# Kernel optimization log

Measured on AMD Instinct MI355X. Metric: run time of the kernel, lower is better.

The kernel has to match this reference:

```python
import jax, jax.numpy as jnp
import numpy as np

B, M, R = 32768, 64, 16

def setup_inputs() -> dict:
    key = jax.random.key(0)
    # x: [B, M, R, 2] real/imag stacked, matching the torch module's input layout
    x = jax.random.normal(key, (B, M, R, 2), dtype=jnp.float32)
    return {"x": x}

def reference(x) -> jnp.ndarray:
    # Combine real/imag channels into a complex matrix per batch element.
    xc = jax.lax.complex(x[..., 0], x[..., 1])  # [B, M, R] complex64
    # Batched reduced QR (replaces the Python loop of per-batch torch.linalg.qr).
    q, _ = jnp.linalg.qr(xc, mode="reduced")    # q: [B, M, R] complex64
    # Split back into stacked real/imag channels: [B, M, R, 2]
    return jnp.stack([q.real, q.imag], axis=-1)
```

## Files before the change

kernel.cpp:

```cpp
#include <hip/hip_runtime.h>


constexpr int Mrows = 64;
constexpr int Rcols = 16;

typedef int v2i __attribute__((ext_vector_type(2)));

#if defined(__has_builtin)
#if __has_builtin(__builtin_amdgcn_permlane16_swap)
#define USE_PL16 1
#else
#define USE_PL16 0
#endif
#if __has_builtin(__builtin_amdgcn_permlane32_swap)
#define USE_PL32 1
#else
#define USE_PL32 0
#endif
#else
#define USE_PL16 0
#define USE_PL32 0
#endif

__device__ __forceinline__ float rdlane(float v, int srclane) {
  return __int_as_float(__builtin_amdgcn_readlane(__float_as_int(v), srclane));
}

__device__ __forceinline__ float plswap16_addf(float v) {
#if USE_PL16
  v2i r = __builtin_amdgcn_permlane16_swap(__float_as_int(v), __float_as_int(v),
                                           false, false);
  return __int_as_float(r[0]) + __int_as_float(r[1]);
#else
  return v + __shfl_xor(v, 16, 64);
#endif
}

__device__ __forceinline__ float plswap32_addf(float v) {
#if USE_PL32
  v2i r = __builtin_amdgcn_permlane32_swap(__float_as_int(v), __float_as_int(v),
                                           false, false);
  return __int_as_float(r[0]) + __int_as_float(r[1]);
#else
  return v + __shfl_xor(v, 32, 64);
#endif
}

template <int CTRL, int RM>
__device__ __forceinline__ double dpp_dadd(double v) {
  union { double d; int i[2]; } u, s;
  u.d = v;
  s.i[0] = __builtin_amdgcn_update_dpp(0, u.i[0], CTRL, RM, 0xF, true);
  s.i[1] = __builtin_amdgcn_update_dpp(0, u.i[1], CTRL, RM, 0xF, true);
  return v + s.d;
}

__device__ __forceinline__ double rdlaned(double v, int srclane) {
  union { double d; int i[2]; } u, r;
  u.d = v;
  r.i[0] = __builtin_amdgcn_readlane(u.i[0], srclane);
  r.i[1] = __builtin_amdgcn_readlane(u.i[1], srclane);
  return r.d;
}

__device__ __forceinline__ double wsum64d_fast(double v) {
  v = dpp_dadd<0xB1, 0xF>(v);
  v = dpp_dadd<0x4E, 0xF>(v);
  v = dpp_dadd<0x141, 0xF>(v);
  v = dpp_dadd<0x140, 0xF>(v);
  v = dpp_dadd<0x142, 0xA>(v);
  v = dpp_dadd<0x143, 0xC>(v);
  return rdlaned(v, 63);
}

__device__ void qr_f64_fused(const float* __restrict__ x,
                             float* __restrict__ out, int b, int lane) {
  const float4* xp = reinterpret_cast<const float4*>(
      x + (size_t)b * (Mrows * Rcols * 2) + (size_t)lane * (Rcols * 2));
  double xr[Rcols], xi[Rcols], ar[Rcols], ai[Rcols];
#pragma unroll
  for (int k = 0; k < Rcols / 2; ++k) {
    float4 t = xp[k];
    xr[2 * k] = (double)t.x;      xi[2 * k] = (double)t.y;
    xr[2 * k + 1] = (double)t.z;  xi[2 * k + 1] = (double)t.w;
  }
#pragma unroll
  for (int j = 0; j < Rcols; ++j) { ar[j] = xr[j]; ai[j] = xi[j]; }

#pragma unroll
  for (int i = 0; i < Rcols; ++i) {
    double cr = ar[i], ci = ai[i];
    double sq = (lane > i) ? (cr * cr + ci * ci) : 0.0;
    double xnorm2 = wsum64d_fast(sq);
    double alphr = rdlaned(cr, i);
    double alphi = rdlaned(ci, i);

    double tr, ti;
    if (xnorm2 == 0.0 && alphi == 0.0) {
      tr = 0.0;  ti = 0.0;
    } else {
      double nrm = sqrt(alphr * alphr + alphi * alphi + xnorm2);
      double beta = (alphr >= 0.0) ? -nrm : nrm;
      double rb = 1.0 / beta;
      tr = (beta - alphr) * rb;
      ti = -alphi * rb;
      double dr = alphr - beta, di = alphi;
      double inv = 1.0 / (dr * dr + di * di);
      double sr = dr * inv, si = -di * inv;
      if (lane > i) {
        double nr = cr * sr - ci * si;
        double ni = cr * si + ci * sr;
        ar[i] = nr;
        ai[i] = ni;
      }
      if (lane == i) { ar[i] = beta; ai[i] = 0.0; }
    }

    double vr = (lane == i) ? 1.0 : ((lane > i) ? ar[i] : 0.0);
    double vi = (lane == i) ? 0.0 : ((lane > i) ? ai[i] : 0.0);
    const double ctr = tr, cti = -ti;
#pragma unroll
    for (int j = i + 1; j < Rcols; ++j) {
      double pr = fma(vr, ar[j], vi * ai[j]);
      double pi = fma(vr, ai[j], -(vi * ar[j]));
      pr = wsum64d_fast(pr);
      pi = wsum64d_fast(pi);
      double wr = fma(ctr, pr, -(cti * pi));
      double wi = fma(ctr, pi, cti * pr);
      ar[j] = fma(-wr, vr, fma(wi, vi, ar[j]));
      ai[j] = fma(-wr, vi, fma(-wi, vr, ai[j]));
    }

    double swr = xr[i], swi = xi[i];
#pragma unroll
    for (int k = 0; k < Rcols; ++k) {
      if (k >= i) break;
      double rr = rdlaned(ar[i], k);
      double ri = rdlaned(ai[i], k);
      swr = fma(-xr[k], rr, fma(xi[k], ri, swr));
      swi = fma(-xr[k], ri, fma(-xi[k], rr, swi));
    }
    double rbd = 1.0 / rdlaned(ar[i], i);
    xr[i] = swr * rbd;
    xi[i] = swi * rbd;
  }

  float4* op = reinterpret_cast<float4*>(
      out + (size_t)b * (Mrows * Rcols * 2) + (size_t)lane * (Rcols * 2));
#pragma unroll
  for (int k = 0; k < Rcols / 2; ++k) {
    op[k] = make_float4((float)xr[2 * k], (float)xi[2 * k],
                        (float)xr[2 * k + 1], (float)xi[2 * k + 1]);
  }
}

template <int I>
__device__ __forceinline__ void qr_step(int lane, float (&Ar)[16], float (&Ai)[16],
                                        float (&Pr)[16], float (&Pi)[16],
                                        int bpaR, bool& risky) {
  const int c = lane & 15;
  const bool g0 = (lane < 16);

  float ahi = 0.f, alo = 0.f;
#pragma unroll
  for (int m = 0; m < 16; ++m) {
    float s = fmaf(Ar[m], Ar[m], Ai[m] * Ai[m]);
    if (m > I) ahi += s; else alo += s;
  }
  float locn = g0 ? ahi : (ahi + alo);
  locn = plswap16_addf(locn);
  locn = plswap32_addf(locn);
  float xnorm2 = rdlane(locn, I);
  float alphr = rdlane(Ar[I], I);
  float alphi = rdlane(Ai[I], I);
  risky = risky || (fabsf(alphr) < 2e-4f);

  float ctr, cti, dr, di, beta_s;
  if (xnorm2 == 0.f && alphi == 0.f) {
    ctr = 0.f; cti = 0.f; dr = 0.f; di = 0.f;
    beta_s = alphr;
  } else {
    float nrm = __builtin_amdgcn_sqrtf(
        fmaf(alphr, alphr, fmaf(alphi, alphi, xnorm2)));
    float beta = (alphr >= 0.f) ? -nrm : nrm;
    float rbeta = __builtin_amdgcn_rcpf(beta);
    float tr = (beta - alphr) * rbeta;
    float ti = -alphi * rbeta;
    dr = alphr - beta;  di = alphi;
    float inv = __builtin_amdgcn_rcpf(fmaf(dr, dr, di * di));
    ctr = tr * inv;
    cti = -(ti * inv);
    beta_s = beta;
  }
  float rbq = __builtin_amdgcn_rcpf(beta_s);

  float ur[16], ui[16];
#pragma unroll
  for (int m = 0; m < 16; ++m) {
    ur[m] = __int_as_float(__builtin_amdgcn_ds_swizzle(
        __float_as_int(Ar[m]), (I << 5) | 0x10));
    ui[m] = __int_as_float(__builtin_amdgcn_ds_swizzle(
        __float_as_int(Ai[m]), (I << 5) | 0x10));
  }
#pragma unroll
  for (int m = 0; m < I; ++m) {
    ur[m] = g0 ? 0.f : ur[m];
    ui[m] = g0 ? 0.f : ui[m];
  }
  ur[I] = g0 ? dr : ur[I];
  ui[I] = g0 ? di : ui[I];

  float pr = 0.f, pi = 0.f;
#pragma unroll
  for (int m = 0; m < 16; ++m) {
    pr = fmaf(ur[m], Ar[m], fmaf(ui[m], Ai[m], pr));
    pi = fmaf(ur[m], Ai[m], fmaf(-ui[m], Ar[m], pi));
  }
  pr = plswap16_addf(pr);  pr = plswap32_addf(pr);
  pi = plswap16_addf(pi);  pi = plswap32_addf(pi);
  const bool cle = (c <= I);
  pr = cle ? 0.f : pr;
  pi = cle ? 0.f : pi;

  float wr = fmaf(ctr, pr, -(cti * pi));
  float wi = fmaf(ctr, pi, cti * pr);
#pragma unroll
  for (int m = 0; m < 16; ++m) {
    Ar[m] = fmaf(-wr, ur[m], fmaf(wi, ui[m], Ar[m]));
    Ai[m] = fmaf(-wr, ui[m], fmaf(-wi, ur[m], Ai[m]));
  }

  float rr = __int_as_float(
      __builtin_amdgcn_ds_bpermute(bpaR, __float_as_int(Ar[I])));
  float ri = __int_as_float(
      __builtin_amdgcn_ds_bpermute(bpaR, __float_as_int(Ai[I])));
  const bool ceq = (c == I);
  const bool clt = (c < I);
  rr = ceq ? (beta_s - 1.f) : rr;
  rr = clt ? 0.f : rr;
  ri = cle ? 0.f : ri;

#pragma unroll
  for (int m = 0; m < 16; ++m) {
    ur[m] = __int_as_float(__builtin_amdgcn_ds_swizzle(
        __float_as_int(Pr[m]), (I << 5) | 0x10));
    ui[m] = __int_as_float(__builtin_amdgcn_ds_swizzle(
        __float_as_int(Pi[m]), (I << 5) | 0x10));
  }
#pragma unroll
  for (int m = 0; m < 16; ++m) {
    float qbr = ur[m] * rbq;
    float qbi = ui[m] * rbq;
    Pr[m] = fmaf(-qbr, rr, fmaf(qbi, ri, Pr[m]));
    Pi[m] = fmaf(-qbr, ri, fmaf(-qbi, rr, Pi[m]));
  }
}

__global__ __launch_bounds__(256)
__attribute__((amdgpu_waves_per_eu(3)))
void qr_fused(const float* __restrict__ x, float* __restrict__ out, int B) {
  const int lane = threadIdx.x & 63;
  const int wave = threadIdx.x >> 6;
  const int b = blockIdx.x * 4 + wave;
  if (b >= B) return;
  const int c = lane & 15;
  const int gbase = lane & 48;
  const int bpaR = c << 2;

  const float2* xp = reinterpret_cast<const float2*>(x) +
                     (size_t)b * (Mrows * Rcols) + (size_t)gbase * Rcols + c;
  float Ar[16], Ai[16], Pr[16], Pi[16];
#pragma unroll
  for (int m = 0; m < 16; ++m) {
    float2 t = xp[m * Rcols];
    Ar[m] = t.x;  Ai[m] = t.y;
    Pr[m] = t.x;  Pi[m] = t.y;
  }

  bool risky = false;
  qr_step<0>(lane, Ar, Ai, Pr, Pi, bpaR, risky);
  qr_step<1>(lane, Ar, Ai, Pr, Pi, bpaR, risky);
  qr_step<2>(lane, Ar, Ai, Pr, Pi, bpaR, risky);
  qr_step<3>(lane, Ar, Ai, Pr, Pi, bpaR, risky);
  qr_step<4>(lane, Ar, Ai, Pr, Pi, bpaR, risky);
  qr_step<5>(lane, Ar, Ai, Pr, Pi, bpaR, risky);
  qr_step<6>(lane, Ar, Ai, Pr, Pi, bpaR, risky);
  qr_step<7>(lane, Ar, Ai, Pr, Pi, bpaR, risky);
  qr_step<8>(lane, Ar, Ai, Pr, Pi, bpaR, risky);
  qr_step<9>(lane, Ar, Ai, Pr, Pi, bpaR, risky);
  qr_step<10>(lane, Ar, Ai, Pr, Pi, bpaR, risky);
  qr_step<11>(lane, Ar, Ai, Pr, Pi, bpaR, risky);
  qr_step<12>(lane, Ar, Ai, Pr, Pi, bpaR, risky);
  qr_step<13>(lane, Ar, Ai, Pr, Pi, bpaR, risky);
  qr_step<14>(lane, Ar, Ai, Pr, Pi, bpaR, risky);
  qr_step<15>(lane, Ar, Ai, Pr, Pi, bpaR, risky);

  if (risky) {
    qr_f64_fused(x, out, b, lane);
    return;
  }

  float2* op = reinterpret_cast<float2*>(out) +
               (size_t)b * (Mrows * Rcols) + (size_t)gbase * Rcols + c;
#pragma unroll
  for (int m = 0; m < 16; ++m) {
    op[m * Rcols] = make_float2(Pr[m], Pi[m]);
  }
}

extern "C" void kernel_launch(void* const* d_in, const int* in_sizes, int n_in,
                              void* d_out, int out_size, void* d_ws,
                              size_t ws_size, hipStream_t stream) {
  const float* x = (const float*)d_in[0];
  float* out = (float*)d_out;
  const int B = in_sizes[0] / (Mrows * Rcols * 2);
  dim3 block(256);
  dim3 grid((B + 3) / 4);
  qr_fused<<<grid, block, 0, stream>>>(x, out, B);
}
```

Measured before the change: 585.6 us.

## Pack QR step arithmetic into float2 FMAs and downdate column norms incrementally

Stores the per-lane matrix and Q registers as two-wide float vectors so the dot product, rank-1 update and Q update can compile to packed FMA instructions. It also replaces the per-step recomputation of the column norm (a 16-element reduction plus two cross-lane swaps) with a running column sum-of-squares. That sum is computed once up front and downdated each step by the squared R entry. The downdate can lose accuracy through cancellation, which is only partly guarded by clamping at zero and by the existing fp64 fallback.

```diff
diff --git a/kernel.cpp b/kernel.cpp
--- a/kernel.cpp
+++ b/kernel.cpp
@@ -5,6 +5,7 @@
 constexpr int Rcols = 16;
 
 typedef int v2i __attribute__((ext_vector_type(2)));
+typedef float v2f __attribute__((ext_vector_type(2)));
 
 #if defined(__has_builtin)
 #if __has_builtin(__builtin_amdgcn_permlane16_swap)
@@ -44,6 +45,24 @@
 #else
   return v + __shfl_xor(v, 32, 64);
 #endif
+}
+
+__device__ __forceinline__ v2f pkfma(v2f a, v2f b, v2f c) {
+#if defined(__has_builtin) && __has_builtin(__builtin_elementwise_fma)
+  return __builtin_elementwise_fma(a, b, c);
+#else
+  v2f r;
+  r[0] = fmaf(a[0], b[0], c[0]);
+  r[1] = fmaf(a[1], b[1], c[1]);
+  return r;
+#endif
+}
+
+__device__ __forceinline__ v2f splat2(float s) { v2f r; r[0] = s; r[1] = s; return r; }
+
+template <int IMM>
+__device__ __forceinline__ float dswz(float v) {
+  return __int_as_float(__builtin_amdgcn_ds_swizzle(__float_as_int(v), IMM));
 }
 
 template <int CTRL, int RM>
@@ -155,24 +174,21 @@
 }
 
 template <int I>
-__device__ __forceinline__ void qr_step(int lane, float (&Ar)[16], float (&Ai)[16],
-                                        float (&Pr)[16], float (&Pi)[16],
-                                        int bpaR, bool& risky) {
+__device__ __forceinline__ void qr_step(int lane,
+                                        v2f (&Ar2)[8], v2f (&Ai2)[8],
+                                        v2f (&Pr2)[8], v2f (&Pi2)[8],
+                                        float& S, int bpaR, bool& risky) {
   const int c = lane & 15;
   const bool g0 = (lane < 16);
-
-  float ahi = 0.f, alo = 0.f;
-#pragma unroll
-  for (int m = 0; m < 16; ++m) {
-    float s = fmaf(Ar[m], Ar[m], Ai[m] * Ai[m]);
-    if (m > I) ahi += s; else alo += s;
-  }
-  float locn = g0 ? ahi : (ahi + alo);
-  locn = plswap16_addf(locn);
-  locn = plswap32_addf(locn);
-  float xnorm2 = rdlane(locn, I);
-  float alphr = rdlane(Ar[I], I);
-  float alphi = rdlane(Ai[I], I);
+  constexpr int IH = I / 2;
+  constexpr int ILo = I % 2;
+  constexpr int SWZ = (I << 5) | 0x10;
+  const v2f z2 = splat2(0.f);
+
+  float alphr = rdlane(Ar2[IH][ILo], I);
+  float alphi = rdlane(Ai2[IH][ILo], I);
+  float SI = rdlane(S, I);
+  float xnorm2 = fmaxf(SI - fmaf(alphr, alphr, alphi * alphi), 0.f);
   risky = risky || (fabsf(alphr) < 2e-4f);
 
   float ctr, cti, dr, di, beta_s;
@@ -194,28 +210,39 @@
   }
   float rbq = __builtin_amdgcn_rcpf(beta_s);
 
-  float ur[16], ui[16];
-#pragma unroll
-  for (int m = 0; m < 16; ++m) {
-    ur[m] = __int_as_float(__builtin_amdgcn_ds_swizzle(
-        __float_as_int(Ar[m]), (I << 5) | 0x10));
-    ui[m] = __int_as_float(__builtin_amdgcn_ds_swizzle(
-        __float_as_int(Ai[m]), (I << 5) | 0x10));
-  }
-#pragma unroll
-  for (int m = 0; m < I; ++m) {
-    ur[m] = g0 ? 0.f : ur[m];
-    ui[m] = g0 ? 0.f : ui[m];
-  }
-  ur[I] = g0 ? dr : ur[I];
-  ui[I] = g0 ? di : ui[I];
-
-  float pr = 0.f, pi = 0.f;
-#pragma unroll
-  for (int m = 0; m < 16; ++m) {
-    pr = fmaf(ur[m], Ar[m], fmaf(ui[m], Ai[m], pr));
-    pi = fmaf(ur[m], Ai[m], fmaf(-ui[m], Ar[m], pi));
-  }
+  v2f ur2[8], ui2[8];
+#pragma unroll
+  for (int h = 0; h < 8; ++h) {
+    v2f t, s;
+    t[0] = dswz<SWZ>(Ar2[h][0]);
+    t[1] = dswz<SWZ>(Ar2[h][1]);
+    s[0] = dswz<SWZ>(Ai2[h][0]);
+    s[1] = dswz<SWZ>(Ai2[h][1]);
+    ur2[h] = t;  ui2[h] = s;
+  }
+#pragma unroll
+  for (int h = 0; h < IH; ++h) {
+    ur2[h] = g0 ? z2 : ur2[h];
+    ui2[h] = g0 ? z2 : ui2[h];
+  }
+  if constexpr (ILo == 1) {
+    ur2[IH][0] = g0 ? 0.f : ur2[IH][0];
+    ui2[IH][0] = g0 ? 0.f : ui2[IH][0];
+    ur2[IH][1] = g0 ? dr : ur2[IH][1];
+    ui2[IH][1] = g0 ? di : ui2[IH][1];
+  } else {
+    ur2[IH][0] = g0 ? dr : ur2[IH][0];
+    ui2[IH][0] = g0 ? di : ui2[IH][0];
+  }
+
+  v2f prv = z2, piv = z2;
+#pragma unroll
+  for (int h = 0; h < 8; ++h) {
+    prv = pkfma(ur2[h], Ar2[h], pkfma(ui2[h], Ai2[h], prv));
+    piv = pkfma(ur2[h], Ai2[h], pkfma(-ui2[h], Ar2[h], piv));
+  }
+  float pr = prv[0] + prv[1];
+  float pi = piv[0] + piv[1];
   pr = plswap16_addf(pr);  pr = plswap32_addf(pr);
   pi = plswap16_addf(pi);  pi = plswap32_addf(pi);
   const bool cle = (c <= I);
@@ -224,35 +251,41 @@
 
   float wr = fmaf(ctr, pr, -(cti * pi));
   float wi = fmaf(ctr, pi, cti * pr);
-#pragma unroll
-  for (int m = 0; m < 16; ++m) {
-    Ar[m] = fmaf(-wr, ur[m], fmaf(wi, ui[m], Ar[m]));
-    Ai[m] = fmaf(-wr, ui[m], fmaf(-wi, ur[m], Ai[m]));
+  const v2f wrv = splat2(wr), wiv = splat2(wi);
+#pragma unroll
+  for (int h = 0; h < 8; ++h) {
+    Ar2[h] = pkfma(-wrv, ur2[h], pkfma(wiv, ui2[h], Ar2[h]));
+    Ai2[h] = pkfma(-wrv, ui2[h], pkfma(-wiv, ur2[h], Ai2[h]));
   }
 
   float rr = __int_as_float(
-      __builtin_amdgcn_ds_bpermute(bpaR, __float_as_int(Ar[I])));
+      __builtin_amdgcn_ds_bpermute(bpaR, __float_as_int(Ar2[IH][ILo])));
   float ri = __int_as_float(
-      __builtin_amdgcn_ds_bpermute(bpaR, __float_as_int(Ai[I])));
+      __builtin_amdgcn_ds_bpermute(bpaR, __float_as_int(Ai2[IH][ILo])));
   const bool ceq = (c == I);
   const bool clt = (c < I);
   rr = ceq ? (beta_s - 1.f) : rr;
   rr = clt ? 0.f : rr;
   ri = cle ? 0.f : ri;
 
-#pragma unroll
-  for (int m = 0; m < 16; ++m) {
-    ur[m] = __int_as_float(__builtin_amdgcn_ds_swizzle(
-        __float_as_int(Pr[m]), (I << 5) | 0x10));
-    ui[m] = __int_as_float(__builtin_amdgcn_ds_swizzle(
-        __float_as_int(Pi[m]), (I << 5) | 0x10));
-  }
-#pragma unroll
-  for (int m = 0; m < 16; ++m) {
-    float qbr = ur[m] * rbq;
-    float qbi = ui[m] * rbq;
-    Pr[m] = fmaf(-qbr, rr, fmaf(qbi, ri, Pr[m]));
-    Pi[m] = fmaf(-qbr, ri, fmaf(-qbi, rr, Pi[m]));
+  S = S - fmaf(rr, rr, ri * ri);
+
+  const v2f rrv = splat2(rr * rbq), riv = splat2(ri * rbq);
+
+  v2f br2[8], bi2[8];
+#pragma unroll
+  for (int h = 0; h < 8; ++h) {
+    v2f t, s;
+    t[0] = dswz<SWZ>(Pr2[h][0]);
+    t[1] = dswz<SWZ>(Pr2[h][1]);
+    s[0] = dswz<SWZ>(Pi2[h][0]);
+    s[1] = dswz<SWZ>(Pi2[h][1]);
+    br2[h] = t;  bi2[h] = s;
+  }
+#pragma unroll
+  for (int h = 0; h < 8; ++h) {
+    Pr2[h] = pkfma(-br2[h], rrv, pkfma(bi2[h], riv, Pr2[h]));
+    Pi2[h] = pkfma(-br2[h], riv, pkfma(-bi2[h], rrv, Pi2[h]));
   }
 }
 
@@ -269,31 +302,44 @@
 
   const float2* xp = reinterpret_cast<const float2*>(x) +
                      (size_t)b * (Mrows * Rcols) + (size_t)gbase * Rcols + c;
-  float Ar[16], Ai[16], Pr[16], Pi[16];
-#pragma unroll
-  for (int m = 0; m < 16; ++m) {
-    float2 t = xp[m * Rcols];
-    Ar[m] = t.x;  Ai[m] = t.y;
-    Pr[m] = t.x;  Pi[m] = t.y;
-  }
+  v2f Ar2[8], Ai2[8], Pr2[8], Pi2[8];
+#pragma unroll
+  for (int h = 0; h < 8; ++h) {
+    float2 t0 = xp[(2 * h) * Rcols];
+    float2 t1 = xp[(2 * h + 1) * Rcols];
+    v2f r, s;
+    r[0] = t0.x;  r[1] = t1.x;
+    s[0] = t0.y;  s[1] = t1.y;
+    Ar2[h] = r;  Ai2[h] = s;
+    Pr2[h] = r;  Pi2[h] = s;
+  }
+
+  v2f s2 = splat2(0.f);
+#pragma unroll
+  for (int h = 0; h < 8; ++h) {
+    s2 = pkfma(Ar2[h], Ar2[h], pkfma(Ai2[h], Ai2[h], s2));
+  }
+  float S = s2[0] + s2[1];
+  S = plswap16_addf(S);
+  S = plswap32_addf(S);
 
   bool risky = false;
-  qr_step<0>(lane, Ar, Ai, Pr, Pi, bpaR, risky);
-  qr_step<1>(lane, Ar, Ai, Pr, Pi, bpaR, risky);
-  qr_step<2>(lane, Ar, Ai, Pr, Pi, bpaR, risky);
-  qr_step<3>(lane, Ar, Ai, Pr, Pi, bpaR, risky);
-  qr_step<4>(lane, Ar, Ai, Pr, Pi, bpaR, risky);
-  qr_step<5>(lane, Ar, Ai, Pr, Pi, bpaR, risky);
-  qr_step<6>(lane, Ar, Ai, Pr, Pi, bpaR, risky);
-  qr_step<7>(lane, Ar, Ai, Pr, Pi, bpaR, risky);
-  qr_step<8>(lane, Ar, Ai, Pr, Pi, bpaR, risky);
-  qr_step<9>(lane, Ar, Ai, Pr, Pi, bpaR, risky);
-  qr_step<10>(lane, Ar, Ai, Pr, Pi, bpaR, risky);
-  qr_step<11>(lane, Ar, Ai, Pr, Pi, bpaR, risky);
-  qr_step<12>(lane, Ar, Ai, Pr, Pi, bpaR, risky);
-  qr_step<13>(lane, Ar, Ai, Pr, Pi, bpaR, risky);
-  qr_step<14>(lane, Ar, Ai, Pr, Pi, bpaR, risky);
-  qr_step<15>(lane, Ar, Ai, Pr, Pi, bpaR, risky);
+  qr_step<0>(lane, Ar2, Ai2, Pr2, Pi2, S, bpaR, risky);
+  qr_step<1>(lane, Ar2, Ai2, Pr2, Pi2, S, bpaR, risky);
+  qr_step<2>(lane, Ar2, Ai2, Pr2, Pi2, S, bpaR, risky);
+  qr_step<3>(lane, Ar2, Ai2, Pr2, Pi2, S, bpaR, risky);
+  qr_step<4>(lane, Ar2, Ai2, Pr2, Pi2, S, bpaR, risky);
+  qr_step<5>(lane, Ar2, Ai2, Pr2, Pi2, S, bpaR, risky);
+  qr_step<6>(lane, Ar2, Ai2, Pr2, Pi2, S, bpaR, risky);
+  qr_step<7>(lane, Ar2, Ai2, Pr2, Pi2, S, bpaR, risky);
+  qr_step<8>(lane, Ar2, Ai2, Pr2, Pi2, S, bpaR, risky);
+  qr_step<9>(lane, Ar2, Ai2, Pr2, Pi2, S, bpaR, risky);
+  qr_step<10>(lane, Ar2, Ai2, Pr2, Pi2, S, bpaR, risky);
+  qr_step<11>(lane, Ar2, Ai2, Pr2, Pi2, S, bpaR, risky);
+  qr_step<12>(lane, Ar2, Ai2, Pr2, Pi2, S, bpaR, risky);
+  qr_step<13>(lane, Ar2, Ai2, Pr2, Pi2, S, bpaR, risky);
+  qr_step<14>(lane, Ar2, Ai2, Pr2, Pi2, S, bpaR, risky);
+  qr_step<15>(lane, Ar2, Ai2, Pr2, Pi2, S, bpaR, risky);
 
   if (risky) {
     qr_f64_fused(x, out, b, lane);
@@ -303,8 +349,9 @@
   float2* op = reinterpret_cast<float2*>(out) +
                (size_t)b * (Mrows * Rcols) + (size_t)gbase * Rcols + c;
 #pragma unroll
-  for (int m = 0; m < 16; ++m) {
-    op[m * Rcols] = make_float2(Pr[m], Pi[m]);
+  for (int h = 0; h < 8; ++h) {
+    op[(2 * h) * Rcols] = make_float2(Pr2[h][0], Pi2[h][0]);
+    op[(2 * h + 1) * Rcols] = make_float2(Pr2[h][1], Pi2[h][1]);
   }
 }
 
```

Result: faster. 551.9 us (-5.7%).
